# Performance work log

Measured on AMD Instinct MI355X. Metric: run time of the kernel, lower is better.

Reference implementation:

```python
import jax, jax.numpy as jnp
import numpy as np

# FP4 e2m1 lookup: nibble -> value (bit3 = sign, bits2:0 = e2m1 magnitude)
FP4_LUT = jnp.array([0.0, 0.5, 1.0, 1.5, 2.0, 3.0, 4.0, 6.0,
                     -0.0, -0.5, -1.0, -1.5, -2.0, -3.0, -4.0, -6.0], dtype=jnp.float32)
BLOCK = 16  # elements per micro-scale (one uint8 E8M0 scale per 16 fp4 values)


def _dequant(packed, sf):
    """packed: [R, K//2] int bytes (two fp4 nibbles each, low nibble first).
    sf: [R, K//16] E8M0 exponents (value = 2^(sf-127)). Returns [R, K] f32."""
    R, Kh = packed.shape
    K = Kh * 2
    lo = packed & 0xF
    hi = (packed >> 4) & 0xF
    nib = jnp.stack([lo, hi], axis=-1).reshape(R, K)
    vals = FP4_LUT[nib]  # [R, K]
    block_scale = jnp.exp2((sf - 127).astype(jnp.float32))  # [R, K//16]
    return (vals.reshape(R, K // BLOCK, BLOCK) * block_scale[:, :, None]).reshape(R, K)


def setup_inputs() -> dict:
    key = jax.random.key(0)
    ks = jax.random.split(key, 6)
    M, N, K = 8192, 4096, 4224  # K = in_features(4096) + select_num(128)
    A_packed = jax.random.randint(ks[0], (M, K // 2), 0, 256, dtype=jnp.int32)
    SFA = jax.random.randint(ks[1], (M, K // BLOCK), 118, 134, dtype=jnp.int32)
    B_packed = jax.random.randint(ks[2], (N, K // 2), 0, 256, dtype=jnp.int32)
    SFB = jax.random.randint(ks[3], (N, K // BLOCK), 118, 134, dtype=jnp.int32)
    scale = jax.random.uniform(ks[4], (1,), dtype=jnp.float32, minval=0.5, maxval=1.5)
    bias = jax.random.normal(ks[5], (N,), dtype=jnp.float32)
    return {"A_packed": A_packed, "SFA": SFA, "scale": scale,
            "B_packed": B_packed, "SFB": SFB, "bias": bias}


def reference(A_packed, SFA, scale, B_packed, SFB, bias):
    A = _dequant(A_packed, SFA)        # [M, K]
    B = _dequant(B_packed, SFB)        # [N, K]
    # y = scale * (A @ B^T) + bias   (self.scale == 1.0 folded into scale)
    y = scale[0] * jnp.einsum('mk,nk->mn', A, B) + bias[None, :]
    return y
```

## Files before the change

kernel.cpp:

```cpp
#include <hip/hip_runtime.h>
#include <stdint.h>

#define M_DIM 8192
#define N_DIM 4096
#define K_DIM 4224
#define BK 64

typedef float f32x16 __attribute__((ext_vector_type(16)));
typedef int   i32x8  __attribute__((ext_vector_type(8)));
typedef int   i32x4  __attribute__((ext_vector_type(4)));

__device__ __forceinline__ uint32_t conv4(uint32_t x, uint32_t k1) {
    uint32_t n7   = x & 0x07070707u;
    uint32_t base = __builtin_amdgcn_perm(0x46444240u, 0x3E3C3800u, n7);
    uint32_t nz   = __builtin_amdgcn_perm(0x01010101u, 0x01010100u, n7);
    uint32_t sign = (x & 0x08080808u) << 4;
    return (base + nz * k1 - (nz << 6)) | sign;
}

__global__ __launch_bounds__(256) void dequant_all(
    const int* __restrict__ Ap, const int* __restrict__ SFA, uint8_t* __restrict__ Aout,
    const int* __restrict__ Bp, const int* __restrict__ SFB, uint8_t* __restrict__ Bout)
{
    const int nblkA = M_DIM * K_DIM / 16;
    int i = blockIdx.x * 256 + threadIdx.x;
    const int* p; const int* sf; uint8_t* out; int idx;
    if (i < nblkA) { p = Ap; sf = SFA; out = Aout; idx = i; }
    else           { p = Bp; sf = SFB; out = Bout; idx = i - nblkA; }

    const int4* p4 = (const int4*)p;
    int4 p0 = p4[2 * idx];
    int4 p1 = p4[2 * idx + 1];
    int s4 = (sf[idx] - 127) << 2;
    uint32_t k1 = (uint32_t)(s4 + 64);

    uint32_t o[4];
#pragma unroll
    for (int g = 0; g < 2; ++g) {
        int4 pg = g ? p1 : p0;
        uint32_t w = (uint32_t)(pg.x & 0xFF) | ((uint32_t)(pg.y & 0xFF) << 8) |
                     ((uint32_t)(pg.z & 0xFF) << 16) | ((uint32_t)pg.w << 24);
        uint32_t lr = conv4(w & 0x0F0F0F0Fu, k1);
        uint32_t hr = conv4((w >> 4) & 0x0F0F0F0Fu, k1);
        o[2 * g]     = __builtin_amdgcn_perm(hr, lr, 0x05010400u);
        o[2 * g + 1] = __builtin_amdgcn_perm(hr, lr, 0x07030602u);
    }
    *(uint4*)(out + (size_t)idx * 16) = make_uint4(o[0], o[1], o[2], o[3]);
}

__global__ __launch_bounds__(256) void gemm_mx(
    const uint8_t* __restrict__ A, const uint8_t* __restrict__ B,
    const float* __restrict__ scale, const float* __restrict__ bias,
    float* __restrict__ C)
{
    __shared__ uint8_t smem[16384];
    uint8_t* As = smem;
    uint8_t* Bs = smem + 8192;

    const int tid  = threadIdx.x;
    const int lane = tid & 63;
    const int w    = tid >> 6;
    const int wm   = w >> 1;
    const int wn   = w & 1;
    const int r31  = lane & 31;
    const int h    = lane >> 5;

    const int bn0 = blockIdx.x * 128;
    const int bm0 = blockIdx.y * 128;

    f32x16 acc[2][2];
#pragma unroll
    for (int i = 0; i < 2; ++i)
#pragma unroll
        for (int j = 0; j < 2; ++j)
            acc[i][j] = (f32x16)(0.0f);

    const int srow = lane >> 2;
    const int scol = (((lane & 3) ^ ((lane >> 3) & 3)) << 4);
    const uint8_t* Ag = A + (size_t)(bm0 + w * 32 + srow) * K_DIM + scol;
    const uint8_t* Bg = B + (size_t)(bn0 + w * 32 + srow) * K_DIM + scol;
    uint8_t* Asw = As + w * 2048;
    uint8_t* Bsw = Bs + w * 2048;

    const int sx = (r31 >> 1) & 3;
    const uint8_t* pa_lo[2]; const uint8_t* pa_hi[2];
    const uint8_t* pb_lo[2]; const uint8_t* pb_hi[2];
#pragma unroll
    for (int mi = 0; mi < 2; ++mi) {
        const uint8_t* base = As + (wm * 64 + mi * 32 + r31) * 64;
        pa_lo[mi] = base + (((2 * h)     ^ sx) << 4);
        pa_hi[mi] = base + (((2 * h + 1) ^ sx) << 4);
    }
#pragma unroll
    for (int ni = 0; ni < 2; ++ni) {
        const uint8_t* base = Bs + (wn * 64 + ni * 32 + r31) * 64;
        pb_lo[ni] = base + (((2 * h)     ^ sx) << 4);
        pb_hi[ni] = base + (((2 * h + 1) ^ sx) << 4);
    }

    for (int kt = 0; kt < K_DIM / BK; ++kt) {
        const uint8_t* ag = Ag + kt * BK;
        const uint8_t* bg = Bg + kt * BK;
        __syncthreads();
        __builtin_amdgcn_global_load_lds(
            (const __attribute__((address_space(1))) void*)(ag),
            (__attribute__((address_space(3))) void*)(Asw), 16, 0, 0);
        __builtin_amdgcn_global_load_lds(
            (const __attribute__((address_space(1))) void*)(ag + (size_t)16 * K_DIM),
            (__attribute__((address_space(3))) void*)(Asw + 1024), 16, 0, 0);
        __builtin_amdgcn_global_load_lds(
            (const __attribute__((address_space(1))) void*)(bg),
            (__attribute__((address_space(3))) void*)(Bsw), 16, 0, 0);
        __builtin_amdgcn_global_load_lds(
            (const __attribute__((address_space(1))) void*)(bg + (size_t)16 * K_DIM),
            (__attribute__((address_space(3))) void*)(Bsw + 1024), 16, 0, 0);
        __syncthreads();

        i32x8 af[2], bf[2];
#pragma unroll
        for (int mi = 0; mi < 2; ++mi) {
            i32x4 lo = *(const i32x4*)pa_lo[mi];
            i32x4 hi = *(const i32x4*)pa_hi[mi];
            af[mi] = __builtin_shufflevector(lo, hi, 0, 1, 2, 3, 4, 5, 6, 7);
        }
#pragma unroll
        for (int ni = 0; ni < 2; ++ni) {
            i32x4 lo = *(const i32x4*)pb_lo[ni];
            i32x4 hi = *(const i32x4*)pb_hi[ni];
            bf[ni] = __builtin_shufflevector(lo, hi, 0, 1, 2, 3, 4, 5, 6, 7);
        }

#pragma unroll
        for (int mi = 0; mi < 2; ++mi)
#pragma unroll
            for (int ni = 0; ni < 2; ++ni)
                acc[mi][ni] = __builtin_amdgcn_mfma_scale_f32_32x32x64_f8f6f4(
                    af[mi], bf[ni], acc[mi][ni],
                    1, 1,
                    0, 0x7F7F7F7F,
                    0, 0x7F7F7F7F);
    }

    const float sc = scale[0];
#pragma unroll
    for (int ni = 0; ni < 2; ++ni) {
        const int col = bn0 + wn * 64 + ni * 32 + r31;
        const float bv = bias[col];
#pragma unroll
        for (int mi = 0; mi < 2; ++mi) {
            const int rbase = bm0 + wm * 64 + mi * 32 + 4 * h;
#pragma unroll
            for (int reg = 0; reg < 16; ++reg) {
                const int row = rbase + (reg & 3) + 8 * (reg >> 2);
                C[(size_t)row * N_DIM + col] = sc * acc[mi][ni][reg] + bv;
            }
        }
    }
}

extern "C" void kernel_launch(void* const* d_in, const int* in_sizes, int n_in,
                              void* d_out, int out_size, void* d_ws, size_t ws_size,
                              hipStream_t stream) {
    const int*   A_packed = (const int*)d_in[0];
    const int*   SFA      = (const int*)d_in[1];
    const float* scale    = (const float*)d_in[2];
    const int*   B_packed = (const int*)d_in[3];
    const int*   SFB      = (const int*)d_in[4];
    const float* bias     = (const float*)d_in[5];
    float*       out      = (float*)d_out;

    uint8_t* Abf8 = (uint8_t*)d_ws;
    uint8_t* Bbf8 = Abf8 + (size_t)M_DIM * K_DIM;

    const int nblkA = M_DIM * K_DIM / 16;
    const int nblkB = N_DIM * K_DIM / 16;
    dequant_all<<<(nblkA + nblkB) / 256, 256, 0, stream>>>(
        A_packed, SFA, Abf8, B_packed, SFB, Bbf8);

    dim3 grid(N_DIM / 128, M_DIM / 128);
    gemm_mx<<<grid, 256, 0, stream>>>(Abf8, Bbf8, scale, bias, out);
}
```

Before: 385.0 us.

## Double-buffer LDS tiles with async prefetch and manual vmcnt waits in GEMM

```diff
diff --git a/kernel.cpp b/kernel.cpp
--- a/kernel.cpp
+++ b/kernel.cpp
@@ -9,6 +9,10 @@
 typedef float f32x16 __attribute__((ext_vector_type(16)));
 typedef int   i32x8  __attribute__((ext_vector_type(8)));
 typedef int   i32x4  __attribute__((ext_vector_type(4)));
+
+#define RAW_BARRIER()  asm volatile("s_barrier" ::: "memory")
+#define WAIT_VM4()     asm volatile("s_waitcnt vmcnt(4)" ::: "memory")
+#define WAIT_VM0()     asm volatile("s_waitcnt vmcnt(0)" ::: "memory")
 
 __device__ __forceinline__ uint32_t conv4(uint32_t x, uint32_t k1) {
     uint32_t n7   = x & 0x07070707u;
@@ -53,7 +57,7 @@
     const float* __restrict__ scale, const float* __restrict__ bias,
     float* __restrict__ C)
 {
-    __shared__ uint8_t smem[16384];
+    __shared__ uint8_t smem[32768];
     uint8_t* As = smem;
     uint8_t* Bs = smem + 8192;
 
@@ -82,6 +86,24 @@
     uint8_t* Asw = As + w * 2048;
     uint8_t* Bsw = Bs + w * 2048;
 
+#define STAGE(koff, boff)                                                        \
+    do {                                                                         \
+        const uint8_t* ag_ = Ag + (koff);                                        \
+        const uint8_t* bg_ = Bg + (koff);                                        \
+        __builtin_amdgcn_global_load_lds(                                        \
+            (const __attribute__((address_space(1))) void*)(ag_),                \
+            (__attribute__((address_space(3))) void*)(Asw + (boff)), 16, 0, 0);  \
+        __builtin_amdgcn_global_load_lds(                                        \
+            (const __attribute__((address_space(1))) void*)(ag_ + (size_t)16 * K_DIM), \
+            (__attribute__((address_space(3))) void*)(Asw + (boff) + 1024), 16, 0, 0); \
+        __builtin_amdgcn_global_load_lds(                                        \
+            (const __attribute__((address_space(1))) void*)(bg_),                \
+            (__attribute__((address_space(3))) void*)(Bsw + (boff)), 16, 0, 0);  \
+        __builtin_amdgcn_global_load_lds(                                        \
+            (const __attribute__((address_space(1))) void*)(bg_ + (size_t)16 * K_DIM), \
+            (__attribute__((address_space(3))) void*)(Bsw + (boff) + 1024), 16, 0, 0); \
+    } while (0)
+
     const int sx = (r31 >> 1) & 3;
     const uint8_t* pa_lo[2]; const uint8_t* pa_hi[2];
     const uint8_t* pb_lo[2]; const uint8_t* pb_hi[2];
@@ -98,38 +120,20 @@
         pb_hi[ni] = base + (((2 * h + 1) ^ sx) << 4);
     }
 
-    for (int kt = 0; kt < K_DIM / BK; ++kt) {
-        const uint8_t* ag = Ag + kt * BK;
-        const uint8_t* bg = Bg + kt * BK;
-        __syncthreads();
-        __builtin_amdgcn_global_load_lds(
-            (const __attribute__((address_space(1))) void*)(ag),
-            (__attribute__((address_space(3))) void*)(Asw), 16, 0, 0);
-        __builtin_amdgcn_global_load_lds(
-            (const __attribute__((address_space(1))) void*)(ag + (size_t)16 * K_DIM),
-            (__attribute__((address_space(3))) void*)(Asw + 1024), 16, 0, 0);
-        __builtin_amdgcn_global_load_lds(
-            (const __attribute__((address_space(1))) void*)(bg),
-            (__attribute__((address_space(3))) void*)(Bsw), 16, 0, 0);
-        __builtin_amdgcn_global_load_lds(
-            (const __attribute__((address_space(1))) void*)(bg + (size_t)16 * K_DIM),
-            (__attribute__((address_space(3))) void*)(Bsw + 1024), 16, 0, 0);
-        __syncthreads();
-
+    auto compute = [&](int off) {
         i32x8 af[2], bf[2];
 #pragma unroll
         for (int mi = 0; mi < 2; ++mi) {
-            i32x4 lo = *(const i32x4*)pa_lo[mi];
-            i32x4 hi = *(const i32x4*)pa_hi[mi];
+            i32x4 lo = *(const i32x4*)(pa_lo[mi] + off);
+            i32x4 hi = *(const i32x4*)(pa_hi[mi] + off);
             af[mi] = __builtin_shufflevector(lo, hi, 0, 1, 2, 3, 4, 5, 6, 7);
         }
 #pragma unroll
         for (int ni = 0; ni < 2; ++ni) {
-            i32x4 lo = *(const i32x4*)pb_lo[ni];
-            i32x4 hi = *(const i32x4*)pb_hi[ni];
+            i32x4 lo = *(const i32x4*)(pb_lo[ni] + off);
+            i32x4 hi = *(const i32x4*)(pb_hi[ni] + off);
             bf[ni] = __builtin_shufflevector(lo, hi, 0, 1, 2, 3, 4, 5, 6, 7);
         }
-
 #pragma unroll
         for (int mi = 0; mi < 2; ++mi)
 #pragma unroll
@@ -139,7 +143,28 @@
                     1, 1,
                     0, 0x7F7F7F7F,
                     0, 0x7F7F7F7F);
-    }
+    };
+
+    const int NT = K_DIM / BK;
+    STAGE(0, 0);
+    for (int kt = 0; kt < NT; kt += 2) {
+        STAGE((kt + 1) * BK, 16384);
+        WAIT_VM4();
+        RAW_BARRIER();
+        compute(0);
+        RAW_BARRIER();
+
+        if (kt + 2 < NT) {
+            STAGE((kt + 2) * BK, 0);
+            WAIT_VM4();
+        } else {
+            WAIT_VM0();
+        }
+        RAW_BARRIER();
+        compute(16384);
+        RAW_BARRIER();
+    }
+#undef STAGE
 
     const float sc = scale[0];
 #pragma unroll
```

After: 370.7 us. 3.7% less time.
